# Performance work log

Measured on AMD Instinct MI355X. Metric: run time of the kernel, lower is better.

## Reference

```python
import jax, jax.numpy as jnp
import numpy as np

DIM = 1024
HEADS = 16
HEAD_DIM = DIM // HEADS
D_FF = 4 * DIM
EPS = 1e-5


def _layernorm(x, g, b):
    mu = jnp.mean(x, axis=-1, keepdims=True)
    var = jnp.mean(jnp.square(x - mu), axis=-1, keepdims=True)
    return (x - mu) * jax.lax.rsqrt(var + EPS) * g + b


def setup_inputs() -> dict:
    key = jax.random.key(0)
    ks = jax.random.split(key, 8)
    s = 0.02
    return {
        "x": jax.random.normal(ks[0], (2, 2048, DIM), dtype=jnp.float32),
        "Wqkv": jax.random.normal(ks[1], (DIM, 3 * DIM), dtype=jnp.float32) * s,
        "bqkv": jnp.zeros((3 * DIM,), dtype=jnp.float32),
        "Wout": jax.random.normal(ks[2], (DIM, DIM), dtype=jnp.float32) * s,
        "bout": jnp.zeros((DIM,), dtype=jnp.float32),
        "W1": jax.random.normal(ks[3], (DIM, D_FF), dtype=jnp.float32) * s,
        "b1": jnp.zeros((D_FF,), dtype=jnp.float32),
        "W2": jax.random.normal(ks[4], (D_FF, DIM), dtype=jnp.float32) * s,
        "b2": jnp.zeros((DIM,), dtype=jnp.float32),
        "g1": jnp.ones((DIM,), dtype=jnp.float32),
        "be1": jnp.zeros((DIM,), dtype=jnp.float32),
        "g2": jnp.ones((DIM,), dtype=jnp.float32),
        "be2": jnp.zeros((DIM,), dtype=jnp.float32),
    }


def reference(x, Wqkv, bqkv, Wout, bout, W1, b1, W2, b2, g1, be1, g2, be2):
    B, T, C = x.shape
    # --- multi-head self-attention (explicit QK^T softmax, no mask/cache) ---
    qkv = (x @ Wqkv + bqkv).reshape(B, T, 3, HEADS, HEAD_DIM)
    q = qkv[:, :, 0].transpose(0, 2, 1, 3)  # (B,H,T,hd)
    k = qkv[:, :, 1].transpose(0, 2, 1, 3)
    v = qkv[:, :, 2].transpose(0, 2, 1, 3)
    scale = HEAD_DIM ** -0.5
    scores = jnp.einsum("bhqd,bhkd->bhqk", q, k) * scale  # (B,H,T,T)
    attn = jax.nn.softmax(scores, axis=-1)
    o = jnp.einsum("bhqk,bhkd->bhqd", attn, v)
    o = o.transpose(0, 2, 1, 3).reshape(B, T, C)
    attn_out = o @ Wout + bout
    # --- Post-LN: LN applied to sublayer output, then residual ---
    x = x + _layernorm(attn_out, g1, be1)
    # --- FFN with exact GELU ---
    h = jax.nn.gelu(x @ W1 + b1, approximate=False)
    ffn_out = h @ W2 + b2
    x = x + _layernorm(ffn_out, g2, be2)
    return x
```

## Files before the change

### kernel.cpp

```cpp
#include <hip/hip_runtime.h>
#include <cstdint>
#include <cstddef>

#define DIM 1024
#define HEADS 16
#define HD 64
#define DFF 4096
#define TSEQ 2048
#define EPS 1e-5f

#define WAITCNT_VM4 0xF74
#define WAITCNT_VM0 0xF70
#define WAITCNT_VM8 0xF78
#define WAITCNT_LGKM0 0xC07F

typedef __bf16 bf16x8 __attribute__((ext_vector_type(8)));
typedef __bf16 bf16x4 __attribute__((ext_vector_type(4)));
typedef float floatx4 __attribute__((ext_vector_type(4)));

__device__ __forceinline__ unsigned short f2bf(float f) {
  union { float f; unsigned int u; } v; v.f = f;
  return (unsigned short)((v.u + 0x7FFFu + ((v.u >> 16) & 1u)) >> 16);
}

__device__ __forceinline__ float exp2_fast(float x) {
#if __has_builtin(__builtin_amdgcn_exp2f)
  return __builtin_amdgcn_exp2f(x);
#else
  float r;
  asm("v_exp_f32 %0, %1" : "=v"(r) : "v"(x));
  return r;
#endif
}

__device__ __forceinline__ float gelu_f(float v) {
  const float u = v * (0.7978845608f + 0.0356774081f * v * v);
  const float e = __expf(2.0f * u);
  const float t = 1.0f - 2.0f / (e + 1.0f);
  return 0.5f * v * (1.0f + t);
}

__device__ __forceinline__ void async16(const void* g, void* l) {
  __builtin_amdgcn_global_load_lds(
      (const __attribute__((address_space(1))) void*)g,
      (__attribute__((address_space(3))) void*)l, 16, 0, 0);
}

__global__ __launch_bounds__(256) void prep_all(const float* __restrict__ x,
                                                const float* __restrict__ Wqkv,
                                                const float* __restrict__ Wout,
                                                const float* __restrict__ W1,
                                                const float* __restrict__ W2,
                                                unsigned short* __restrict__ xb,
                                                unsigned short* __restrict__ WqkvT,
                                                unsigned short* __restrict__ WoutT,
                                                unsigned short* __restrict__ W1T,
                                                unsigned short* __restrict__ W2T) {
  const int bid = blockIdx.x;
  const int tid = threadIdx.x;
  if (bid < 4096) {
    const int i = bid * 256 + tid;
    float4 v = ((const float4*)x)[i];
    ushort4 o;
    o.x = f2bf(v.x); o.y = f2bf(v.y); o.z = f2bf(v.z); o.w = f2bf(v.w);
    ((ushort4*)xb)[i] = o;
    return;
  }
  int id = bid - 4096;
  const float* src; unsigned short* dst; int R, C, gx;
  if (id < 3072)      {            src = Wqkv; dst = WqkvT; R = 1024; C = 3072; gx = 96; }
  else if (id < 4096) { id -= 3072; src = Wout; dst = WoutT; R = 1024; C = 1024; gx = 32; }
  else if (id < 8192) { id -= 4096; src = W1;   dst = W1T;   R = 1024; C = 4096; gx = 128; }
  else                { id -= 8192; src = W2;   dst = W2T;   R = 4096; C = 1024; gx = 32; }
  const int c0 = (id % gx) * 32, r0 = (id / gx) * 32;
  const int tx = tid & 31, ty = tid >> 5;
  __shared__ float tile[32][33];
#pragma unroll
  for (int i = 0; i < 32; i += 8)
    tile[ty + i][tx] = src[(size_t)(r0 + ty + i) * C + c0 + tx];
  __syncthreads();
#pragma unroll
  for (int i = 0; i < 32; i += 8)
    dst[(size_t)(c0 + ty + i) * R + r0 + tx] = f2bf(tile[tx][ty + i]);
}

#define PIPELINED_KLOOP3(NIT)                                                        \
  auto issue = [&](int s, int k0) {                                                  \
    async16(Ab0 + k0, &lds[s][tid * 8]);                                             \
    async16(Ab1 + k0, &lds[s][2048 + tid * 8]);                                      \
    async16(Bb0 + k0, &lds[s][4096 + tid * 8]);                                      \
    async16(Bb1 + k0, &lds[s][6144 + tid * 8]);                                      \
  };                                                                                 \
  issue(0, 0);                                                                       \
  issue(1, 32);                                                                      \
  int sidx = 0;                                                                      \
  for (int k = 0; k < (NIT); k++) {                                                  \
    if (k < (NIT)-1) __builtin_amdgcn_s_waitcnt(WAITCNT_VM4);                        \
    else             __builtin_amdgcn_s_waitcnt(WAITCNT_VM0);                        \
    __builtin_amdgcn_s_barrier();                                                    \
    if (k + 2 < (NIT)) {                                                             \
      int s2 = sidx + 2; if (s2 >= 3) s2 -= 3;                                       \
      issue(s2, (k + 2) * 32);                                                       \
    }                                                                                \
    bf16x8 af[4], bg[4];                                                             \
    _Pragma("unroll")                                                                \
    for (int mi = 0; mi < 4; mi++)                                                   \
      af[mi] = *(const bf16x8*)&lds[sidx][(wm + mi * 16 + l16) * 32 + quad * 8];     \
    _Pragma("unroll")                                                                \
    for (int ni = 0; ni < 4; ni++)                                                   \
      bg[ni] = *(const bf16x8*)&lds[sidx][4096 + (wn + ni * 16 + l16) * 32 + quad * 8]; \
    _Pragma("unroll")                                                                \
    for (int mi = 0; mi < 4; mi++)                                                   \
      _Pragma("unroll")                                                              \
      for (int ni = 0; ni < 4; ni++)                                                 \
        acc[mi][ni] =                                                                \
            __builtin_amdgcn_mfma_f32_16x16x32_bf16(af[mi], bg[ni], acc[mi][ni], 0, 0, 0); \
    sidx = (sidx == 2) ? 0 : sidx + 1;                                               \
  }

#define PIPELINED_KLOOP2(NIT)                                                        \
  auto issue = [&](int s, int k0) {                                                  \
    async16(Ab0 + k0, &lds[s][tid * 8]);                                             \
    async16(Ab1 + k0, &lds[s][2048 + tid * 8]);                                      \
    async16(Bb0 + k0, &lds[s][4096 + tid * 8]);                                      \
    async16(Bb1 + k0, &lds[s][6144 + tid * 8]);                                      \
  };                                                                                 \
  issue(0, 0);                                                                       \
  int sidx = 0;                                                                      \
  for (int k = 0; k < (NIT); k++) {                                                  \
    if (k + 1 < (NIT)) {                                                             \
      issue(sidx ^ 1, (k + 1) * 32);                                                 \
      __builtin_amdgcn_s_waitcnt(WAITCNT_VM4);                                       \
    } else {                                                                         \
      __builtin_amdgcn_s_waitcnt(WAITCNT_VM0);                                       \
    }                                                                                \
    __builtin_amdgcn_s_barrier();                                                    \
    bf16x8 af[4], bg[4];                                                             \
    _Pragma("unroll")                                                                \
    for (int mi = 0; mi < 4; mi++)                                                   \
      af[mi] = *(const bf16x8*)&lds[sidx][(wm + mi * 16 + l16) * 32 + quad * 8];     \
    _Pragma("unroll")                                                                \
    for (int ni = 0; ni < 4; ni++)                                                   \
      bg[ni] = *(const bf16x8*)&lds[sidx][4096 + (wn + ni * 16 + l16) * 32 + quad * 8]; \
    _Pragma("unroll")                                                                \
    for (int mi = 0; mi < 4; mi++)                                                   \
      _Pragma("unroll")                                                              \
      for (int ni = 0; ni < 4; ni++)                                                 \
        acc[mi][ni] =                                                                \
            __builtin_amdgcn_mfma_f32_16x16x32_bf16(af[mi], bg[ni], acc[mi][ni], 0, 0, 0); \
    __builtin_amdgcn_s_waitcnt(WAITCNT_LGKM0);                                       \
    __builtin_amdgcn_s_barrier();                                                    \
    sidx ^= 1;                                                                       \
  }

template <int EPI>
__global__ __launch_bounds__(256) void gemm_bt(const unsigned short* __restrict__ A,
                                               const unsigned short* __restrict__ Bt,
                                               const float* __restrict__ bias,
                                               void* __restrict__ Cout,
                                               int M, int N, int K) {
  __shared__ unsigned short lds[2][8192];
  const int tid = threadIdx.x;
  int bxx = blockIdx.x, byy = blockIdx.y;
  if (gridDim.x == 32 && gridDim.y == 32) {
    const int id = byy * 32 + bxx;
    const int xcd = id & 7, sub = id >> 3;
    bxx = (xcd & 3) * 8 + (sub & 7);
    byy = (xcd >> 2) * 16 + (sub >> 3);
  }
  const int bm = byy * 128, bn = bxx * 128;
  const int wave = tid >> 6, lane = tid & 63;
  const int l16 = lane & 15, quad = lane >> 4;
  const int wm = (wave >> 1) * 64, wn = (wave & 1) * 64;

  floatx4 acc[4][4] = {};

  const int srow = tid >> 2;
  const int scol = (tid & 3) * 8;

  const unsigned short* Ab0 = A + (size_t)(bm + srow) * K + scol;
  const unsigned short* Ab1 = A + (size_t)(bm + 64 + srow) * K + scol;
  const unsigned short* Bb0 = Bt + (size_t)(bn + srow) * K + scol;
  const unsigned short* Bb1 = Bt + (size_t)(bn + 64 + srow) * K + scol;

  const int nit = K >> 5;
  PIPELINED_KLOOP2(nit)
  __syncthreads();

  if (EPI == 0) {
#pragma unroll
    for (int ni = 0; ni < 4; ni++) {
      const int col = bn + wn + ni * 16 + l16;
      const float bv = bias[col];
#pragma unroll
      for (int mi = 0; mi < 4; mi++) {
        const int row0 = bm + wm + mi * 16 + quad * 4;
#pragma unroll
        for (int r = 0; r < 4; r++)
          ((float*)Cout)[(size_t)(row0 + r) * N + col] = acc[mi][ni][r] + bv;
      }
    }
  } else {
    unsigned short* eb = &lds[0][wave * 1152];
    float bvv[4];
#pragma unroll
    for (int ni = 0; ni < 4; ni++) bvv[ni] = bias[bn + wn + ni * 16 + l16];
    const int lrow = lane >> 2, ck = lane & 3;
#pragma unroll
    for (int mi = 0; mi < 4; mi++) {
#pragma unroll
      for (int ni = 0; ni < 4; ni++)
#pragma unroll
        for (int r = 0; r < 4; r++)
          eb[(quad * 4 + r) * 72 + ni * 16 + l16] =
              f2bf(gelu_f(acc[mi][ni][r] + bvv[ni]));
      __syncthreads();
      unsigned short* gp =
          (unsigned short*)Cout + (size_t)(bm + wm + mi * 16 + lrow) * N + bn + wn;
#pragma unroll
      for (int j = 0; j < 2; j++)
        *(uint4*)(gp + j * 32 + ck * 8) = *(const uint4*)&eb[lrow * 72 + j * 32 + ck * 8];
      __syncthreads();
    }
  }
}

__global__ __launch_bounds__(256) void gemm_splitk(const unsigned short* __restrict__ A,
                                                   const unsigned short* __restrict__ Bt,
                                                   float* __restrict__ Cp,
                                                   int M, int N, int Ktot, int Ksl) {
  __shared__ unsigned short lds[3][8192];
  const int tid = threadIdx.x;
  const int id = (blockIdx.z * 32 + blockIdx.y) * 8 + blockIdx.x;
  const int xcd = id & 7, sub = id >> 3;
  const int bxx = sub & 7;
  const int byz = xcd * (gridDim.z * 4) + (sub >> 3);
  const int byy = byz & 31, bz = byz >> 5;
  const int bm = byy * 128, bn = bxx * 128;
  const int koff = bz * Ksl;
  const int wave = tid >> 6, lane = tid & 63;
  const int l16 = lane & 15, quad = lane >> 4;
  const int wm = (wave >> 1) * 64, wn = (wave & 1) * 64;

  floatx4 acc[4][4] = {};

  const int srow = tid >> 2;
  const int scol = (tid & 3) * 8;

  const unsigned short* Ab0 = A + (size_t)(bm + srow) * Ktot + koff + scol;
  const unsigned short* Ab1 = A + (size_t)(bm + 64 + srow) * Ktot + koff + scol;
  const unsigned short* Bb0 = Bt + (size_t)(bn + srow) * Ktot + koff + scol;
  const unsigned short* Bb1 = Bt + (size_t)(bn + 64 + srow) * Ktot + koff + scol;

  const int nit = Ksl >> 5;
  PIPELINED_KLOOP3(nit)

  float* out = Cp + (size_t)bz * M * (size_t)N;
#pragma unroll
  for (int ni = 0; ni < 4; ni++) {
    const int col = bn + wn + ni * 16 + l16;
#pragma unroll
    for (int mi = 0; mi < 4; mi++) {
      const int row0 = bm + wm + mi * 16 + quad * 4;
#pragma unroll
      for (int r = 0; r < 4; r++)
        out[(size_t)(row0 + r) * N + col] = acc[mi][ni][r];
    }
  }
}

__global__ __launch_bounds__(256) void gemm_qkv(const unsigned short* __restrict__ A,
                                                const unsigned short* __restrict__ Bt,
                                                const float* __restrict__ bias,
                                                unsigned short* __restrict__ Qg,
                                                unsigned short* __restrict__ Kg,
                                                unsigned short* __restrict__ Vtg) {
  const int K = 1024;
  __shared__ unsigned short lds[3][8192];
  const int tid = threadIdx.x;
  const int id = blockIdx.y * 24 + blockIdx.x;
  const int xcd = id & 7, sub = id >> 3;
  const int bxx = (xcd & 3) * 6 + sub % 6;
  const int byy = (xcd >> 2) * 16 + sub / 6;
  const int bm = byy * 128, bn = bxx * 128;
  const int wave = tid >> 6, lane = tid & 63;
  const int l16 = lane & 15, quad = lane >> 4;
  const int wm = (wave >> 1) * 64, wn = (wave & 1) * 64;

  floatx4 acc[4][4] = {};

  const int srow = tid >> 2;
  const int scol = (tid & 3) * 8;

  const unsigned short* Ab0 = A + (size_t)(bm + srow) * K + scol;
  const unsigned short* Ab1 = A + (size_t)(bm + 64 + srow) * K + scol;
  const unsigned short* Bb0 = Bt + (size_t)(bn + srow) * K + scol;
  const unsigned short* Bb1 = Bt + (size_t)(bn + 64 + srow) * K + scol;

  const int nit = K >> 5;
  PIPELINED_KLOOP3(nit)

  const float QSCALE = 0.125f * 1.44269504089f;
#pragma unroll
  for (int ni = 0; ni < 4; ni++) {
    const int col = bn + wn + ni * 16 + l16;
    const float bv = bias[col];
    const int sec = col >> 10;
    const int cc = col & 1023;
    const int hh = cc >> 6, dd = cc & 63;
#pragma unroll
    for (int mi = 0; mi < 4; mi++) {
      const int row0 = bm + wm + mi * 16 + quad * 4;
      const int b2 = row0 >> 11, tt0 = row0 & 2047;
      if (sec == 0) {
        unsigned short* q = Qg + ((size_t)(b2 * HEADS + hh) * TSEQ + tt0) * HD + dd;
#pragma unroll
        for (int r = 0; r < 4; r++)
          q[(size_t)r * HD] = f2bf((acc[mi][ni][r] + bv) * QSCALE);
      } else if (sec == 1) {
        unsigned short* k = Kg + ((size_t)(b2 * HEADS + hh) * TSEQ + tt0) * HD + dd;
#pragma unroll
        for (int r = 0; r < 4; r++)
          k[(size_t)r * HD] = f2bf(acc[mi][ni][r] + bv);
      } else {
        ushort4 o;
        o.x = f2bf(acc[mi][ni][0] + bv);
        o.y = f2bf(acc[mi][ni][1] + bv);
        o.z = f2bf(acc[mi][ni][2] + bv);
        o.w = f2bf(acc[mi][ni][3] + bv);
        *(ushort4*)(Vtg + ((size_t)(b2 * HEADS + hh) * HD + dd) * TSEQ + tt0) = o;
      }
    }
  }
}

__global__ __launch_bounds__(256, 4) void attn_mfma(const unsigned short* __restrict__ Qg,
                                                    const unsigned short* __restrict__ Kg,
                                                    const unsigned short* __restrict__ Vtg,
                                                    unsigned short* __restrict__ ob) {
  __shared__ __align__(16) char smem[40960];
  unsigned short* QPs = (unsigned short*)smem;

  const int bid = blockIdx.x;
  const int lid = (bid & 7) * 128 + (bid >> 3);
  const int qt = lid & 31;
  const int h = (lid >> 5) & 15;
  const int b = lid >> 9;
  const int tid = threadIdx.x;
  const int w = tid >> 6, lane = tid & 63, l16 = lane & 15, quad = lane >> 4;
  const int qg = w >> 1;
  const int kh = w & 1;

  const int r0 = tid >> 3;
  const int c0 = (tid & 7) ^ (r0 & 7);

  const char* Qbase = (const char*)(Qg + ((size_t)(b * HEADS + h) * TSEQ + qt * 64) * HD);
  const char* Kbase = (const char*)(Kg + (size_t)(b * HEADS + h) * TSEQ * HD);
  const char* Vbase = (const char*)(Vtg + (size_t)(b * HEADS + h) * HD * TSEQ);

  auto Ksp = [&](int s) -> char* { return smem + 8192 + s * 8192; };
  auto Vsp = [&](int s) -> char* { return smem + 24576 + s * 8192; };

  auto issueKV = [&](int s, int ch) {
    const size_t koff = (size_t)ch * 64;
#pragma unroll
    for (int i = 0; i < 2; i++) {
      async16(Kbase + (koff + r0 + i * 32) * 128 + c0 * 16, Ksp(s) + (i * 256 + tid) * 16);
      async16(Vbase + (size_t)(r0 + i * 32) * (TSEQ * 2) + koff * 2 + c0 * 16,
              Vsp(s) + (i * 256 + tid) * 16);
    }
  };

#pragma unroll
  for (int i = 0; i < 2; i++)
    async16(Qbase + (size_t)(r0 + i * 32) * 128 + c0 * 16, (char*)QPs + (i * 256 + tid) * 16);
  issueKV(0, 0);
  issueKV(1, 1);

  __builtin_amdgcn_s_waitcnt(WAITCNT_VM8);
  __builtin_amdgcn_s_barrier();

  bf16x8 qf[2][2];
#pragma unroll
  for (int mi = 0; mi < 2; mi++)
#pragma unroll
    for (int kt = 0; kt < 2; kt++) {
      const int row = qg * 32 + mi * 16 + l16;
      qf[mi][kt] = *(const bf16x8*)((const char*)QPs + row * 128 +
                                    (((quad + 4 * kt) ^ (row & 7)) * 16));
    }
  __builtin_amdgcn_s_waitcnt(WAITCNT_LGKM0);
  __builtin_amdgcn_sched_barrier(0);

  union { unsigned short u[8]; bf16x8 b; } onesu;
#pragma unroll
  for (int j = 0; j < 8; j++) onesu.u[j] = 0x3F80;
  const bf16x8 ones = onesu.b;

  floatx4 oacc[2][5] = {};
  char* Pw = (char*)QPs + w * 1152;

  const int NC = TSEQ / 64;
  int sidx = 0;
  for (int ch = 0; ch < NC; ch++) {
    if (ch < NC - 1) __builtin_amdgcn_s_waitcnt(WAITCNT_VM4);
    else             __builtin_amdgcn_s_waitcnt(WAITCNT_VM0);
    __builtin_amdgcn_s_barrier();

    floatx4 sacc[2][2] = {};
    __builtin_amdgcn_s_setprio(1);
#pragma unroll
    for (int kt = 0; kt < 2; kt++) {
#pragma unroll
      for (int ni = 0; ni < 2; ni++) {
        const int krow = kh * 32 + ni * 16 + l16;
        bf16x8 kf = *(const bf16x8*)(Ksp(sidx) + krow * 128 +
                                     (((quad + 4 * kt) ^ (krow & 7)) * 16));
#pragma unroll
        for (int mi = 0; mi < 2; mi++)
          sacc[mi][ni] =
              __builtin_amdgcn_mfma_f32_16x16x32_bf16(qf[mi][kt], kf, sacc[mi][ni], 0, 0, 0);
      }
    }
    __builtin_amdgcn_s_setprio(0);

    bf16x8 pf[2];
#pragma unroll
    for (int mi = 0; mi < 2; mi++) {
#pragma unroll
      for (int ni = 0; ni < 2; ni++)
#pragma unroll
        for (int r = 0; r < 4; r++) {
          const float p = exp2_fast(sacc[mi][ni][r]);
          const unsigned int pu = __builtin_bit_cast(unsigned int, p);
          *((unsigned short*)(Pw + (quad * 4 + r) * 72 + (ni * 16 + l16) * 2)) =
              (unsigned short)(pu >> 16);
        }
      union { bf16x8 v8; bf16x4 v4[2]; } u;
      u.v4[0] = *(const bf16x4*)(Pw + l16 * 72 + quad * 16);
      u.v4[1] = *(const bf16x4*)(Pw + l16 * 72 + quad * 16 + 8);
      pf[mi] = u.v8;
    }

    __builtin_amdgcn_s_setprio(1);
#pragma unroll
    for (int nj = 0; nj < 4; nj++) {
      const int vrow = nj * 16 + l16;
      bf16x8 vf = *(const bf16x8*)(Vsp(sidx) + vrow * 128 +
                                   (((quad + 4 * kh) ^ (vrow & 7)) * 16));
#pragma unroll
      for (int mi = 0; mi < 2; mi++)
        oacc[mi][nj] = __builtin_amdgcn_mfma_f32_16x16x32_bf16(pf[mi], vf, oacc[mi][nj], 0, 0, 0);
    }
#pragma unroll
    for (int mi = 0; mi < 2; mi++)
      oacc[mi][4] = __builtin_amdgcn_mfma_f32_16x16x32_bf16(pf[mi], ones, oacc[mi][4], 0, 0, 0);
    __builtin_amdgcn_s_setprio(0);

    __builtin_amdgcn_s_waitcnt(WAITCNT_LGKM0);
    __builtin_amdgcn_s_barrier();
    if (ch + 2 < NC) issueKV(sidx, ch + 2);
    sidx ^= 1;
  }

  __syncthreads();
  float* Op = (float*)smem + qg * (32 * 66);
  if (kh == 1) {
#pragma unroll
    for (int mi = 0; mi < 2; mi++)
#pragma unroll
      for (int r = 0; r < 4; r++) {
        const int row = mi * 16 + quad * 4 + r;
#pragma unroll
        for (int nj = 0; nj < 4; nj++)
          Op[row * 66 + nj * 16 + l16] = oacc[mi][nj][r];
        if (l16 == 0) Op[row * 66 + 64] = oacc[mi][4][r];
      }
  }
  __syncthreads();
  if (kh == 0) {
#pragma unroll
    for (int mi = 0; mi < 2; mi++)
#pragma unroll
      for (int r = 0; r < 4; r++) {
        const int row = mi * 16 + quad * 4 + r;
        const float inv = 1.0f / (oacc[mi][4][r] + Op[row * 66 + 64]);
        const int t = qt * 64 + qg * 32 + row;
        unsigned short* orow = ob + (size_t)(b * TSEQ + t) * DIM + h * HD + l16;
#pragma unroll
        for (int nj = 0; nj < 4; nj++)
          orow[nj * 16] = f2bf((oacc[mi][nj][r] + Op[row * 66 + nj * 16 + l16]) * inv);
      }
  }
}

template <int NP, int WBF>
__global__ __launch_bounds__(256) void add_ln_red(const float* __restrict__ xin,
                                                  const float* __restrict__ parts,
                                                  const float* __restrict__ bias,
                                                  const float* __restrict__ gw,
                                                  const float* __restrict__ bw,
                                                  float* __restrict__ xout,
                                                  unsigned short* __restrict__ xbf) {
  const size_t MN = (size_t)4096 * DIM;
  const int row = blockIdx.x;
  const int tid = threadIdx.x;
  const int c = tid * 4;
  const size_t base = (size_t)row * DIM;
  float4 v = *(const float4*)(parts + base + c);
#pragma unroll
  for (int p = 1; p < NP; p++) {
    float4 t = *(const float4*)(parts + p * MN + base + c);
    v.x += t.x; v.y += t.y; v.z += t.z; v.w += t.w;
  }
  float4 bb = *(const float4*)(bias + c);
  v.x += bb.x; v.y += bb.y; v.z += bb.z; v.w += bb.w;

  float s = v.x + v.y + v.z + v.w;
  float s2 = v.x * v.x + v.y * v.y + v.z * v.z + v.w * v.w;
#pragma unroll
  for (int off = 1; off < 64; off <<= 1) {
    s += __shfl_xor(s, off);
    s2 += __shfl_xor(s2, off);
  }
  __shared__ float rsum[4], rsq[4];
  if ((tid & 63) == 0) { rsum[tid >> 6] = s; rsq[tid >> 6] = s2; }
  __syncthreads();
  s = rsum[0] + rsum[1] + rsum[2] + rsum[3];
  s2 = rsq[0] + rsq[1] + rsq[2] + rsq[3];
  const float mu = s * (1.0f / DIM);
  const float var = s2 * (1.0f / DIM) - mu * mu;
  const float rstd = rsqrtf(var + EPS);
  float4 xv = *(const float4*)(xin + base + c);
  float4 gv = *(const float4*)(gw + c);
  float4 bv = *(const float4*)(bw + c);
  float4 o;
  o.x = xv.x + (v.x - mu) * rstd * gv.x + bv.x;
  o.y = xv.y + (v.y - mu) * rstd * gv.y + bv.y;
  o.z = xv.z + (v.z - mu) * rstd * gv.z + bv.z;
  o.w = xv.w + (v.w - mu) * rstd * gv.w + bv.w;
  *(float4*)(xout + base + c) = o;
  if (WBF) {
    ushort4 ob;
    ob.x = f2bf(o.x); ob.y = f2bf(o.y); ob.z = f2bf(o.z); ob.w = f2bf(o.w);
    *(ushort4*)(xbf + base + c) = ob;
  }
}

extern "C" void kernel_launch(void* const* d_in, const int* in_sizes, int n_in,
                              void* d_out, int out_size, void* d_ws, size_t ws_size,
                              hipStream_t stream) {
  const float* x    = (const float*)d_in[0];
  const float* Wqkv = (const float*)d_in[1];
  const float* bqkv = (const float*)d_in[2];
  const float* Wout = (const float*)d_in[3];
  const float* bout = (const float*)d_in[4];
  const float* W1   = (const float*)d_in[5];
  const float* b1   = (const float*)d_in[6];
  const float* W2   = (const float*)d_in[7];
  const float* b2   = (const float*)d_in[8];
  const float* g1   = (const float*)d_in[9];
  const float* be1  = (const float*)d_in[10];
  const float* g2   = (const float*)d_in[11];
  const float* be2  = (const float*)d_in[12];

  char* w = (char*)d_ws;
  const size_t MB = 1048576;
  unsigned short* xb     = (unsigned short*)(w + 0 * MB);
  unsigned short* WqkvT  = (unsigned short*)(w + 8 * MB);
  unsigned short* WoutT  = (unsigned short*)(w + 14 * MB);
  unsigned short* W1T    = (unsigned short*)(w + 16 * MB);
  unsigned short* W2T    = (unsigned short*)(w + 24 * MB);
  unsigned short* Qb     = (unsigned short*)(w + 32 * MB);
  unsigned short* Kb     = (unsigned short*)(w + 40 * MB);
  unsigned short* Vtb    = (unsigned short*)(w + 48 * MB);
  unsigned short* obuf   = (unsigned short*)(w + 64 * MB);
  float*          atno_p = (float*)(w + 72 * MB);
  float*          x1     = (float*)(w + 104 * MB);
  unsigned short* x1b    = (unsigned short*)(w + 120 * MB);
  unsigned short* hb     = (unsigned short*)(w + 128 * MB);
  float*          ffn_p  = (float*)(w + 32 * MB);

  prep_all<<<16384, 256, 0, stream>>>(x, Wqkv, Wout, W1, W2, xb, WqkvT, WoutT, W1T, W2T);

  gemm_qkv<<<dim3(24, 32), 256, 0, stream>>>(xb, WqkvT, bqkv, Qb, Kb, Vtb);
  attn_mfma<<<1024, 256, 0, stream>>>(Qb, Kb, Vtb, obuf);
  gemm_splitk<<<dim3(8, 32, 2), 256, 0, stream>>>(obuf, WoutT, atno_p, 4096, 1024, 1024, 512);
  add_ln_red<2, 1><<<4096, 256, 0, stream>>>(x, atno_p, bout, g1, be1, x1, x1b);
  gemm_bt<1><<<dim3(32, 32), 256, 0, stream>>>(x1b, W1T, b1, hb, 4096, 4096, 1024);
  gemm_splitk<<<dim3(8, 32, 2), 256, 0, stream>>>(hb, W2T, ffn_p, 4096, 1024, 4096, 2048);
  add_ln_red<2, 0><<<4096, 256, 0, stream>>>(x1, ffn_p, b2, g2, be2, (float*)d_out, nullptr);
}
```

Baseline: 341.3 us.

## Replace FFN1 GEMM with 256x256-tile, 512-thread kernel using swizzled LDS

The W1 GEMM with GELU epilogue moves from 128x128 tiles with 256 threads to 256x256 tiles with 512 threads (8 waves). Each K-step is 64 wide, double-buffered in 128KB of dynamic LDS, with an XOR swizzle to avoid bank conflicts and s_setprio around the MFMA bursts. The larger tile is meant to raise arithmetic intensity and cut global/LDS traffic per FLOP. The cost is only 256 blocks, which may underfill the CUs, plus higher LDS and register pressure.

```diff
diff --git a/kernel.cpp b/kernel.cpp
--- a/kernel.cpp
+++ b/kernel.cpp
@@ -118,110 +118,116 @@
     sidx = (sidx == 2) ? 0 : sidx + 1;                                               \
   }
 
-#define PIPELINED_KLOOP2(NIT)                                                        \
-  auto issue = [&](int s, int k0) {                                                  \
-    async16(Ab0 + k0, &lds[s][tid * 8]);                                             \
-    async16(Ab1 + k0, &lds[s][2048 + tid * 8]);                                      \
-    async16(Bb0 + k0, &lds[s][4096 + tid * 8]);                                      \
-    async16(Bb1 + k0, &lds[s][6144 + tid * 8]);                                      \
-  };                                                                                 \
-  issue(0, 0);                                                                       \
-  int sidx = 0;                                                                      \
-  for (int k = 0; k < (NIT); k++) {                                                  \
-    if (k + 1 < (NIT)) {                                                             \
-      issue(sidx ^ 1, (k + 1) * 32);                                                 \
-      __builtin_amdgcn_s_waitcnt(WAITCNT_VM4);                                       \
-    } else {                                                                         \
-      __builtin_amdgcn_s_waitcnt(WAITCNT_VM0);                                       \
-    }                                                                                \
-    __builtin_amdgcn_s_barrier();                                                    \
-    bf16x8 af[4], bg[4];                                                             \
-    _Pragma("unroll")                                                                \
-    for (int mi = 0; mi < 4; mi++)                                                   \
-      af[mi] = *(const bf16x8*)&lds[sidx][(wm + mi * 16 + l16) * 32 + quad * 8];     \
-    _Pragma("unroll")                                                                \
-    for (int ni = 0; ni < 4; ni++)                                                   \
-      bg[ni] = *(const bf16x8*)&lds[sidx][4096 + (wn + ni * 16 + l16) * 32 + quad * 8]; \
-    _Pragma("unroll")                                                                \
-    for (int mi = 0; mi < 4; mi++)                                                   \
-      _Pragma("unroll")                                                              \
-      for (int ni = 0; ni < 4; ni++)                                                 \
-        acc[mi][ni] =                                                                \
-            __builtin_amdgcn_mfma_f32_16x16x32_bf16(af[mi], bg[ni], acc[mi][ni], 0, 0, 0); \
-    __builtin_amdgcn_s_waitcnt(WAITCNT_LGKM0);                                       \
-    __builtin_amdgcn_s_barrier();                                                    \
-    sidx ^= 1;                                                                       \
-  }
-
-template <int EPI>
-__global__ __launch_bounds__(256) void gemm_bt(const unsigned short* __restrict__ A,
-                                               const unsigned short* __restrict__ Bt,
-                                               const float* __restrict__ bias,
-                                               void* __restrict__ Cout,
-                                               int M, int N, int K) {
-  __shared__ unsigned short lds[2][8192];
+__global__ __launch_bounds__(512, 2) void gemm256g(const unsigned short* __restrict__ A,
+                                                   const unsigned short* __restrict__ Bt,
+                                                   const float* __restrict__ bias,
+                                                   unsigned short* __restrict__ Cout,
+                                                   int M, int N, int K) {
+  extern __shared__ char smem[];
   const int tid = threadIdx.x;
   int bxx = blockIdx.x, byy = blockIdx.y;
-  if (gridDim.x == 32 && gridDim.y == 32) {
-    const int id = byy * 32 + bxx;
+  {
+    const int id = byy * 16 + bxx;
     const int xcd = id & 7, sub = id >> 3;
-    bxx = (xcd & 3) * 8 + (sub & 7);
-    byy = (xcd >> 2) * 16 + (sub >> 3);
-  }
-  const int bm = byy * 128, bn = bxx * 128;
-  const int wave = tid >> 6, lane = tid & 63;
+    bxx = (xcd & 3) * 4 + (sub & 3);
+    byy = (xcd >> 2) * 8 + (sub >> 2);
+  }
+  const int bm = byy * 256, bn = bxx * 256;
+  const int lane = tid & 63, wv = tid >> 6;
   const int l16 = lane & 15, quad = lane >> 4;
-  const int wm = (wave >> 1) * 64, wn = (wave & 1) * 64;
-
-  floatx4 acc[4][4] = {};
-
-  const int srow = tid >> 2;
-  const int scol = (tid & 3) * 8;
-
-  const unsigned short* Ab0 = A + (size_t)(bm + srow) * K + scol;
-  const unsigned short* Ab1 = A + (size_t)(bm + 64 + srow) * K + scol;
-  const unsigned short* Bb0 = Bt + (size_t)(bn + srow) * K + scol;
-  const unsigned short* Bb1 = Bt + (size_t)(bn + 64 + srow) * K + scol;
-
-  const int nit = K >> 5;
-  PIPELINED_KLOOP2(nit)
+  const int wr = wv >> 2, wc = wv & 3;
+
+  const int srow = tid >> 3;
+  const int scc = (tid & 7) ^ (srow & 7);
+  const unsigned short* Asrc = A + (size_t)(bm + srow) * K + scc * 8;
+  const unsigned short* Bsrc = Bt + (size_t)(bn + srow) * K + scc * 8;
+
+  auto stageKstep = [&](int buf, int kk) {
+    char* dA = smem + buf * 65536;
+    char* dB = dA + 32768;
+#pragma unroll
+    for (int h = 0; h < 2; h++)
+#pragma unroll
+      for (int j = 0; j < 2; j++) {
+        async16(Asrc + (size_t)(h * 128 + 64 * j) * K + kk,
+                dA + h * 16384 + (j * 512 + tid) * 16);
+        async16(Bsrc + (size_t)(h * 128 + 64 * j) * K + kk,
+                dB + h * 16384 + (j * 512 + tid) * 16);
+      }
+  };
+
+  floatx4 acc[8][4] = {};
+
+  stageKstep(0, 0);
+  __builtin_amdgcn_s_waitcnt(WAITCNT_VM0);
+  __builtin_amdgcn_s_barrier();
+
+  const int NG = K >> 6;
+  for (int g = 0; g < NG; g++) {
+    const int p = g & 1;
+    const char* Ab = smem + p * 65536 + wr * 16384;
+    const char* Bb = smem + p * 65536 + 32768 + (wc >> 1) * 16384;
+    bf16x8 bg[4][2];
+#pragma unroll
+    for (int q = 0; q < 4; q++) {
+      if (q == 0) {
+        if (g + 1 < NG) stageKstep(p ^ 1, (g + 1) << 6);
+#pragma unroll
+        for (int ni = 0; ni < 4; ni++) {
+          const int lr = (wc & 1) * 64 + ni * 16 + l16;
+#pragma unroll
+          for (int ks = 0; ks < 2; ks++)
+            bg[ni][ks] = *(const bf16x8*)(Bb + lr * 128 +
+                                          (((quad + 4 * ks) ^ (lr & 7)) * 16));
+        }
+      }
+      bf16x8 af[2][2];
+#pragma unroll
+      for (int m = 0; m < 2; m++) {
+        const int lr = (q * 2 + m) * 16 + l16;
+#pragma unroll
+        for (int ks = 0; ks < 2; ks++)
+          af[m][ks] = *(const bf16x8*)(Ab + lr * 128 +
+                                       (((quad + 4 * ks) ^ (lr & 7)) * 16));
+      }
+      __builtin_amdgcn_s_barrier();
+      __builtin_amdgcn_s_waitcnt(WAITCNT_LGKM0);
+      __builtin_amdgcn_s_setprio(1);
+#pragma unroll
+      for (int ks = 0; ks < 2; ks++)
+#pragma unroll
+        for (int ni = 0; ni < 4; ni++)
+#pragma unroll
+          for (int m = 0; m < 2; m++)
+            acc[q * 2 + m][ni] = __builtin_amdgcn_mfma_f32_16x16x32_bf16(
+                af[m][ks], bg[ni][ks], acc[q * 2 + m][ni], 0, 0, 0);
+      __builtin_amdgcn_s_setprio(0);
+      if (q == 3) __builtin_amdgcn_s_waitcnt(WAITCNT_VM0);
+      __builtin_amdgcn_s_barrier();
+    }
+  }
+
   __syncthreads();
-
-  if (EPI == 0) {
-#pragma unroll
-    for (int ni = 0; ni < 4; ni++) {
-      const int col = bn + wn + ni * 16 + l16;
-      const float bv = bias[col];
-#pragma unroll
-      for (int mi = 0; mi < 4; mi++) {
-        const int row0 = bm + wm + mi * 16 + quad * 4;
-#pragma unroll
-        for (int r = 0; r < 4; r++)
-          ((float*)Cout)[(size_t)(row0 + r) * N + col] = acc[mi][ni][r] + bv;
-      }
-    }
-  } else {
-    unsigned short* eb = &lds[0][wave * 1152];
-    float bvv[4];
-#pragma unroll
-    for (int ni = 0; ni < 4; ni++) bvv[ni] = bias[bn + wn + ni * 16 + l16];
-    const int lrow = lane >> 2, ck = lane & 3;
-#pragma unroll
-    for (int mi = 0; mi < 4; mi++) {
-#pragma unroll
-      for (int ni = 0; ni < 4; ni++)
-#pragma unroll
-        for (int r = 0; r < 4; r++)
-          eb[(quad * 4 + r) * 72 + ni * 16 + l16] =
-              f2bf(gelu_f(acc[mi][ni][r] + bvv[ni]));
-      __syncthreads();
-      unsigned short* gp =
-          (unsigned short*)Cout + (size_t)(bm + wm + mi * 16 + lrow) * N + bn + wn;
-#pragma unroll
-      for (int j = 0; j < 2; j++)
-        *(uint4*)(gp + j * 32 + ck * 8) = *(const uint4*)&eb[lrow * 72 + j * 32 + ck * 8];
-      __syncthreads();
-    }
+  unsigned short* eb = (unsigned short*)smem + wv * 1152;
+  float bvv[4];
+#pragma unroll
+  for (int ni = 0; ni < 4; ni++) bvv[ni] = bias[bn + wc * 64 + ni * 16 + l16];
+  const int lrow = lane >> 2, ck = lane & 3;
+#pragma unroll
+  for (int mi = 0; mi < 8; mi++) {
+#pragma unroll
+    for (int ni = 0; ni < 4; ni++)
+#pragma unroll
+      for (int r = 0; r < 4; r++)
+        eb[(quad * 4 + r) * 72 + ni * 16 + l16] =
+            f2bf(gelu_f(acc[mi][ni][r] + bvv[ni]));
+    __syncthreads();
+    unsigned short* gp =
+        Cout + (size_t)(bm + wr * 128 + mi * 16 + lrow) * N + bn + wc * 64;
+#pragma unroll
+    for (int j = 0; j < 2; j++)
+      *(uint4*)(gp + j * 32 + ck * 8) = *(const uint4*)&eb[lrow * 72 + j * 32 + ck * 8];
+    __syncthreads();
   }
 }
 
@@ -564,6 +570,13 @@
   const float* g2   = (const float*)d_in[11];
   const float* be2  = (const float*)d_in[12];
 
+  static bool s_attr = false;
+  if (!s_attr) {
+    hipFuncSetAttribute((const void*)gemm256g,
+                        hipFuncAttributeMaxDynamicSharedMemorySize, 131072);
+    s_attr = true;
+  }
+
   char* w = (char*)d_ws;
   const size_t MB = 1048576;
   unsigned short* xb     = (unsigned short*)(w + 0 * MB);
@@ -587,7 +600,7 @@
   attn_mfma<<<1024, 256, 0, stream>>>(Qb, Kb, Vtb, obuf);
   gemm_splitk<<<dim3(8, 32, 2), 256, 0, stream>>>(obuf, WoutT, atno_p, 4096, 1024, 1024, 512);
   add_ln_red<2, 1><<<4096, 256, 0, stream>>>(x, atno_p, bout, g1, be1, x1, x1b);
-  gemm_bt<1><<<dim3(32, 32), 256, 0, stream>>>(x1b, W1T, b1, hb, 4096, 4096, 1024);
+  gemm256g<<<dim3(16, 16), 512, 131072, stream>>>(x1b, W1T, b1, hb, 4096, 4096, 1024);
   gemm_splitk<<<dim3(8, 32, 2), 256, 0, stream>>>(hb, W2T, ffn_p, 4096, 1024, 4096, 2048);
   add_ln_red<2, 0><<<4096, 256, 0, stream>>>(x1, ffn_p, b2, g2, be2, (float*)d_out, nullptr);
 }
```

New measurement: 338.3 us, median of 2. Within noise of the previous version (-0.9%).
